# Kernel tuning notes

Hardware: AMD Instinct MI355X
Metric: run time of the kernel (lower is better)

The kernel has to match this reference:

```python
import jax, jax.numpy as jnp
import numpy as np

B, T, C, H = 2, 2048, 1024, 16
HD = C // H  # head dim = 64


def setup_inputs() -> dict:
    key = jax.random.key(0)
    ks = jax.random.split(key, 5)
    s = 1.0 / np.sqrt(C)
    return {
        "x": jax.random.normal(ks[0], (B, T, C), dtype=jnp.float32),
        "W_attn": jax.random.normal(ks[1], (3 * C, C), dtype=jnp.float32) * s,
        "b_attn": jax.random.normal(ks[2], (3 * C,), dtype=jnp.float32) * 0.02,
        "W_proj": jax.random.normal(ks[3], (C, C), dtype=jnp.float32) * s,
        "b_proj": jax.random.normal(ks[4], (C,), dtype=jnp.float32) * 0.02,
    }


def reference(x, W_attn, b_attn, W_proj, b_proj):
    Bx, Tx, Cx = x.shape
    # fused QKV projection (torch Linear: x @ W.T + b)
    qkv = x @ W_attn.T + b_attn                      # [B,T,3C]
    q, k, v = jnp.split(qkv, 3, axis=-1)
    # [B,T,C] -> [B,H,T,hd]
    q = q.reshape(Bx, Tx, H, HD).transpose(0, 2, 1, 3)
    k = k.reshape(Bx, Tx, H, HD).transpose(0, 2, 1, 3)
    v = v.reshape(Bx, Tx, H, HD).transpose(0, 2, 1, 3)
    scale = 1.0 / np.sqrt(HD)
    att = jnp.einsum('bhqd,bhkd->bhqk', q, k) * scale  # [B,H,T,T]
    causal = jnp.tril(jnp.ones((Tx, Tx), dtype=bool))
    att = jnp.where(causal[None, None], att, -jnp.inf)
    att = jax.nn.softmax(att, axis=-1)
    y = jnp.einsum('bhqk,bhkd->bhqd', att, v)          # [B,H,T,hd]
    y = y.transpose(0, 2, 1, 3).reshape(Bx, Tx, Cx)
    return y @ W_proj.T + b_proj
```

## Files before the change

kernel.cpp:

```cpp
#include <hip/hip_runtime.h>

typedef unsigned short ushort_t;
typedef __bf16 bf16x8 __attribute__((ext_vector_type(8)));
typedef float f32x4 __attribute__((ext_vector_type(4)));
typedef unsigned u32x4 __attribute__((ext_vector_type(4)));

__device__ inline ushort_t f2bf(float f) {
  unsigned int u = __builtin_bit_cast(unsigned int, f);
  u += 0x7fff + ((u >> 16) & 1);
  return (ushort_t)(u >> 16);
}

__device__ inline unsigned pk_bf(float a, float b) {
  unsigned r;
  asm("v_cvt_pk_bf16_f32 %0, %1, %2" : "=v"(r) : "v"(a), "v"(b));
  return r;
}

__device__ inline void async_ld16(const ushort_t* g, const ushort_t* l) {
  __builtin_amdgcn_global_load_lds(
      (const __attribute__((address_space(1))) void*)g,
      (__attribute__((address_space(3))) void*)l, 16, 0, 0);
}

template <int IMM>
__device__ inline void waitcnt_barrier() {
  asm volatile("" ::: "memory");
  __builtin_amdgcn_s_waitcnt(IMM);
  __builtin_amdgcn_s_barrier();
  asm volatile("" ::: "memory");
}

__global__ void cvt_all(const float* __restrict__ x, const float* __restrict__ wa,
                        const float* __restrict__ wp, ushort_t* __restrict__ xb,
                        ushort_t* __restrict__ wab, ushort_t* __restrict__ wpb) {
  int i = blockIdx.x * 256 + threadIdx.x;
  const float* src;
  ushort_t* dst;
  int off;
  if (i < 1048576) { src = x; dst = xb; off = i; }
  else if (i < 1835008) { src = wa; dst = wab; off = i - 1048576; }
  else { src = wp; dst = wpb; off = i - 1835008; }
  float4 f = ((const float4*)src)[off];
  unsigned long long p = (unsigned long long)f2bf(f.x)
      | ((unsigned long long)f2bf(f.y) << 16)
      | ((unsigned long long)f2bf(f.z) << 32)
      | ((unsigned long long)f2bf(f.w) << 48);
  ((unsigned long long*)dst)[off] = p;
}

template <int BM, int BN, int IM, int JN, int MODE, int TPB>
__global__ __launch_bounds__(TPB) void gemm_bt(
    const ushort_t* __restrict__ A, const ushort_t* __restrict__ B,
    const float* __restrict__ bias, float* __restrict__ Cf,
    ushort_t* __restrict__ Cb, ushort_t* __restrict__ vtb,
    int M, int N, int K, int ldc, float qscale) {
  constexpr int NWN = BN / (JN * 16);
  constexpr int NL = (BM + BN) * 32 / (TPB * 8);
  constexpr int WIMM = 0x0F70 | NL;
  __shared__ __align__(16) ushort_t As[3][BM * 32];
  __shared__ __align__(16) ushort_t Bs[3][BN * 32];
  const int tid = threadIdx.x;
  const int wave = tid >> 6, lane = tid & 63;
  const int quad = lane >> 4, l16 = lane & 15;
  const int wr = wave / NWN, wc = wave % NWN;
  const int wm = wr * IM * 16, wn = wc * JN * 16;
  const int m0 = blockIdx.y * BM, n0 = blockIdx.x * BN;
  const ushort_t* Ag = A + (size_t)m0 * K;
  const ushort_t* Bg = B + (size_t)n0 * K;
  const int slot = (quad ^ ((l16 >> 1) & 3)) * 8;
  f32x4 acc[IM][JN] = {};

  auto stage = [&](int kt, int bsel) {
    int k0 = kt * 32;
#pragma unroll
    for (int p = 0; p < BM * 4 / TPB; ++p) {
      int ci = p * TPB + tid;
      int row = ci >> 2, ch = (ci & 3) ^ ((ci >> 3) & 3);
      async_ld16(Ag + (size_t)row * K + k0 + ch * 8, As[bsel] + (p * TPB + wave * 64) * 8);
    }
#pragma unroll
    for (int p = 0; p < BN * 4 / TPB; ++p) {
      int ci = p * TPB + tid;
      int row = ci >> 2, ch = (ci & 3) ^ ((ci >> 3) & 3);
      async_ld16(Bg + (size_t)row * K + k0 + ch * 8, Bs[bsel] + (p * TPB + wave * 64) * 8);
    }
  };

  const int KT = K / 32;
  stage(0, 0);
  stage(1, 1);
  for (int kt = 0; kt < KT; ++kt) {
    waitcnt_barrier<WIMM>();
    if (kt + 2 < KT) stage(kt + 2, (kt + 2) % 3);
    const ushort_t* Ac = As[kt % 3];
    const ushort_t* Bc = Bs[kt % 3];
    bf16x8 af[IM], bfr[JN];
#pragma unroll
    for (int i = 0; i < IM; ++i)
      af[i] = *(const bf16x8*)(Ac + (wm + i * 16 + l16) * 32 + slot);
#pragma unroll
    for (int j = 0; j < JN; ++j)
      bfr[j] = *(const bf16x8*)(Bc + (wn + j * 16 + l16) * 32 + slot);
#pragma unroll
    for (int i = 0; i < IM; ++i)
#pragma unroll
      for (int j = 0; j < JN; ++j)
        acc[i][j] = __builtin_amdgcn_mfma_f32_16x16x32_bf16(af[i], bfr[j], acc[i][j], 0, 0, 0);
  }

  if (MODE == 1 && n0 >= 2048) {
#pragma unroll
    for (int j = 0; j < JN; ++j) {
      int col = n0 + wn + j * 16 + l16;
      int cv = col - 2048;
      float bv = bias[col];
      size_t rowbase = ((size_t)(cv >> 6)) * 64 + (cv & 63);
#pragma unroll
      for (int i = 0; i < IM; ++i) {
        int rowb = m0 + wm + i * 16 + quad * 4;
        int bb = rowb >> 11, t = rowb & 2047;
        uint2 pp;
        pp.x = pk_bf(acc[i][j][0] + bv, acc[i][j][1] + bv);
        pp.y = pk_bf(acc[i][j][2] + bv, acc[i][j][3] + bv);
        *(uint2*)(vtb + (((size_t)bb * 1024 + rowbase) * 2048 + t)) = pp;
      }
    }
    return;
  }
#pragma unroll
  for (int j = 0; j < JN; ++j) {
    int col = n0 + wn + j * 16 + l16;
    float bv = bias[col];
    float sc = (MODE == 1 && col < 1024) ? qscale : 1.0f;
#pragma unroll
    for (int i = 0; i < IM; ++i)
#pragma unroll
      for (int r = 0; r < 4; ++r) {
        int row = m0 + wm + i * 16 + quad * 4 + r;
        float v = (acc[i][j][r] + bv) * sc;
        if (MODE == 1)
          Cb[(size_t)row * ldc + col] = f2bf(v);
        else
          Cf[(size_t)row * ldc + col] = v;
      }
  }
}

__global__ __launch_bounds__(512, 4) void flash8(
    const ushort_t* __restrict__ qk, const ushort_t* __restrict__ vt,
    ushort_t* __restrict__ y) {
  __shared__ __align__(16) ushort_t Kb[4][4096];
  __shared__ __align__(16) ushort_t Vb[4][4096];
  const int tid = threadIdx.x, wave = tid >> 6, lane = tid & 63;
  const int quad = lane >> 4, l16 = lane & 15;
  const int r7 = l16 & 7;
  const int fK = (l16 & 3) | (((l16 >> 2) & 1) << 2);
  const int kbase = (16 * (l16 >> 2) + (l16 & 3)) * 64;
  const int xx = blockIdx.x, bh = blockIdx.y;
  const int Q = (bh < 16) ? (15 - xx) : xx;
  const int b = bh >> 4, h = bh & 15;
  const int bT = b * 2048;
  const int qw = Q * 128 + wave * 16;

  bf16x8 qf[2];
  {
    const ushort_t* qrow = qk + (size_t)(bT + qw + l16) * 2048 + h * 64 + quad * 8;
    qf[0] = *(const bf16x8*)(qrow);
    qf[1] = *(const bf16x8*)(qrow + 32);
  }

  auto stage = [&](int kt, int bsel) {
    int k0 = kt * 64;
    int row = tid >> 3;
    int chk = (tid & 7) ^ ((row & 3) | (((row >> 4) & 1) << 2));
    int chv = (tid & 7) ^ (row & 7);
    async_ld16(qk + (size_t)(bT + k0 + row) * 2048 + 1024 + h * 64 + chk * 8,
               Kb[bsel] + wave * 512);
    async_ld16(vt + (size_t)(bh * 64 + row) * 2048 + k0 + chv * 8,
               Vb[bsel] + wave * 512);
  };

  f32x4 o[4] = {};
  float lac0 = 0.f, lac1 = 0.f;
  const int KT = 2 * Q + 2;

  stage(0, 0);
  stage(1, 1);
  if (KT > 2) stage(2, 2);
  for (int kt = 0; kt < KT; ++kt) {
    const int cur = kt & 3;
    int ahead = KT - 1 - kt;
    if (ahead >= 2)      waitcnt_barrier<0x0F74>();
    else if (ahead == 1) waitcnt_barrier<0x0F72>();
    else                 waitcnt_barrier<0x0F70>();
    if (kt + 3 < KT) stage(kt + 3, (kt + 3) & 3);
    const ushort_t* Kc = Kb[cur];
    const ushort_t* Vc = Vb[cur];
    bf16x8 kf[4][2];
#pragma unroll
    for (int j = 0; j < 4; ++j)
#pragma unroll
      for (int ks = 0; ks < 2; ++ks)
        kf[j][ks] = *(const bf16x8*)(Kc + kbase + j * 256 + (((ks * 4 + quad) ^ fK) * 8));
    f32x4 s[4] = {};
#pragma unroll
    for (int ks = 0; ks < 2; ++ks)
#pragma unroll
      for (int j = 0; j < 4; ++j)
        s[j] = __builtin_amdgcn_mfma_f32_16x16x32_bf16(kf[j][ks], qf[ks], s[j], 0, 0, 0);
    if (kt >= KT - 2) {
      int qloc = qw + l16;
#pragma unroll
      for (int j = 0; j < 4; ++j)
#pragma unroll
        for (int r = 0; r < 4; ++r)
          if (kt * 64 + quad * 16 + j * 4 + r > qloc) s[j][r] = -1e30f;
    }
#pragma unroll
    for (int j = 0; j < 4; ++j)
#pragma unroll
      for (int r = 0; r < 4; ++r) {
        float pv = exp2f(s[j][r]);
        s[j][r] = pv;
        if (j & 1) lac1 += pv; else lac0 += pv;
      }
    bf16x8 pf[2];
#pragma unroll
    for (int ks = 0; ks < 2; ++ks) {
      u32x4 w;
      w[0] = pk_bf(s[2 * ks][0], s[2 * ks][1]);
      w[1] = pk_bf(s[2 * ks][2], s[2 * ks][3]);
      w[2] = pk_bf(s[2 * ks + 1][0], s[2 * ks + 1][1]);
      w[3] = pk_bf(s[2 * ks + 1][2], s[2 * ks + 1][3]);
      pf[ks] = __builtin_bit_cast(bf16x8, w);
    }
#pragma unroll
    for (int ks = 0; ks < 2; ++ks)
#pragma unroll
      for (int j = 0; j < 4; ++j) {
        bf16x8 vf = *(const bf16x8*)(Vc + (j * 16 + l16) * 64 + (((ks + 2 * quad) ^ r7) * 8));
        o[j] = __builtin_amdgcn_mfma_f32_16x16x32_bf16(vf, pf[ks], o[j], 0, 0, 0);
      }
  }

  {
    float l = lac0 + lac1;
    l += __shfl_xor(l, 16, 64);
    l += __shfl_xor(l, 32, 64);
    float inv = 1.f / l;
    size_t row = (size_t)(bT + qw + l16);
#pragma unroll
    for (int j = 0; j < 4; ++j) {
      uint2 pp;
      pp.x = pk_bf(o[j][0] * inv, o[j][1] * inv);
      pp.y = pk_bf(o[j][2] * inv, o[j][3] * inv);
      *(uint2*)(y + row * 1024 + h * 64 + j * 16 + quad * 4) = pp;
    }
  }
}

extern "C" void kernel_launch(void* const* d_in, const int* in_sizes, int n_in,
                              void* d_out, int out_size, void* d_ws, size_t ws_size,
                              hipStream_t stream) {
  const float* x  = (const float*)d_in[0];
  const float* Wa = (const float*)d_in[1];
  const float* ba = (const float*)d_in[2];
  const float* Wp = (const float*)d_in[3];
  const float* bp = (const float*)d_in[4];
  float* out = (float*)d_out;
  char* ws = (char*)d_ws;
  ushort_t* xb  = (ushort_t*)(ws);
  ushort_t* Wab = (ushort_t*)(ws + 8388608);
  ushort_t* Wpb = (ushort_t*)(ws + 14680064);
  ushort_t* qkb = (ushort_t*)(ws + 16777216);
  ushort_t* yb  = (ushort_t*)(ws + 33554432);
  ushort_t* vtb = (ushort_t*)(ws + 41943040);

  cvt_all<<<8192, 256, 0, stream>>>(x, Wa, Wp, xb, Wab, Wpb);
  gemm_bt<128, 128, 4, 2, 1, 512><<<dim3(24, 32), 512, 0, stream>>>(
      xb, Wab, ba, nullptr, qkb, vtb, 4096, 3072, 1024, 2048, 0.18033688011112042f);
  flash8<<<dim3(16, 32), 512, 0, stream>>>(qkb, vtb, yb);
  gemm_bt<64, 64, 2, 2, 0, 256><<<dim3(16, 64), 256, 0, stream>>>(
      yb, Wpb, bp, out, nullptr, nullptr, 4096, 1024, 1024, 1024, 1.0f);
}
```

Before: 181.2 us.

## Process two key tiles per barrier with double-buffered superstages in flash kernel

The flash attention loop now groups two 64-key tiles into one superstage. It double-buffers superstages instead of keeping a 4-deep single-tile ring, so there is one barrier and full wait per two tiles instead of one per tile. It also raises wave priority around the compute section with s_setprio. The trade-off is shallower prefetch: the next superstage loads while the current one computes, but a full vmcnt(0) wait can expose latency. LDS use is unchanged.

```diff
diff --git a/kernel.cpp b/kernel.cpp
--- a/kernel.cpp
+++ b/kernel.cpp
@@ -147,11 +147,11 @@
   }
 }
 
-__global__ __launch_bounds__(512, 4) void flash8(
+__global__ __launch_bounds__(512, 4) void flash9(
     const ushort_t* __restrict__ qk, const ushort_t* __restrict__ vt,
     ushort_t* __restrict__ y) {
-  __shared__ __align__(16) ushort_t Kb[4][4096];
-  __shared__ __align__(16) ushort_t Vb[4][4096];
+  __shared__ __align__(16) ushort_t Kb[2][2][4096];
+  __shared__ __align__(16) ushort_t Vb[2][2][4096];
   const int tid = threadIdx.x, wave = tid >> 6, lane = tid & 63;
   const int quad = lane >> 4, l16 = lane & 15;
   const int r7 = l16 & 7;
@@ -170,78 +170,83 @@
     qf[1] = *(const bf16x8*)(qrow + 32);
   }
 
-  auto stage = [&](int kt, int bsel) {
+  auto stage1 = [&](int kt, int bsel, int u) {
     int k0 = kt * 64;
     int row = tid >> 3;
     int chk = (tid & 7) ^ ((row & 3) | (((row >> 4) & 1) << 2));
     int chv = (tid & 7) ^ (row & 7);
     async_ld16(qk + (size_t)(bT + k0 + row) * 2048 + 1024 + h * 64 + chk * 8,
-               Kb[bsel] + wave * 512);
+               Kb[bsel][u] + wave * 512);
     async_ld16(vt + (size_t)(bh * 64 + row) * 2048 + k0 + chv * 8,
-               Vb[bsel] + wave * 512);
+               Vb[bsel][u] + wave * 512);
   };
+  auto stageS = [&](int s, int bsel) { stage1(2 * s, bsel, 0); stage1(2 * s + 1, bsel, 1); };
 
   f32x4 o[4] = {};
   float lac0 = 0.f, lac1 = 0.f;
-  const int KT = 2 * Q + 2;
-
-  stage(0, 0);
-  stage(1, 1);
-  if (KT > 2) stage(2, 2);
-  for (int kt = 0; kt < KT; ++kt) {
-    const int cur = kt & 3;
-    int ahead = KT - 1 - kt;
-    if (ahead >= 2)      waitcnt_barrier<0x0F74>();
-    else if (ahead == 1) waitcnt_barrier<0x0F72>();
-    else                 waitcnt_barrier<0x0F70>();
-    if (kt + 3 < KT) stage(kt + 3, (kt + 3) & 3);
-    const ushort_t* Kc = Kb[cur];
-    const ushort_t* Vc = Vb[cur];
-    bf16x8 kf[4][2];
-#pragma unroll
-    for (int j = 0; j < 4; ++j)
+  const int NS = Q + 1;
+
+  stageS(0, 0);
+  for (int s = 0; s < NS; ++s) {
+    const int cur = s & 1;
+    waitcnt_barrier<0x0F70>();
+    if (s + 1 < NS) stageS(s + 1, cur ^ 1);
+    __builtin_amdgcn_s_setprio(1);
+    bf16x8 pf[2][2];
+#pragma unroll
+    for (int u = 0; u < 2; ++u) {
+      const ushort_t* Kc = Kb[cur][u];
+      const ushort_t* Vc = Vb[cur][u];
+      bf16x8 kf[4][2];
+#pragma unroll
+      for (int j = 0; j < 4; ++j)
+#pragma unroll
+        for (int ks = 0; ks < 2; ++ks)
+          kf[j][ks] = *(const bf16x8*)(Kc + kbase + j * 256 + (((ks * 4 + quad) ^ fK) * 8));
+      f32x4 sr[4] = {};
 #pragma unroll
       for (int ks = 0; ks < 2; ++ks)
-        kf[j][ks] = *(const bf16x8*)(Kc + kbase + j * 256 + (((ks * 4 + quad) ^ fK) * 8));
-    f32x4 s[4] = {};
-#pragma unroll
-    for (int ks = 0; ks < 2; ++ks)
+#pragma unroll
+        for (int j = 0; j < 4; ++j)
+          sr[j] = __builtin_amdgcn_mfma_f32_16x16x32_bf16(kf[j][ks], qf[ks], sr[j], 0, 0, 0);
+      if (s == NS - 1) {
+        int qloc = qw + l16;
+        int kt0 = (2 * s + u) * 64;
+#pragma unroll
+        for (int j = 0; j < 4; ++j)
+#pragma unroll
+          for (int r = 0; r < 4; ++r)
+            if (kt0 + quad * 16 + j * 4 + r > qloc) sr[j][r] = -1e30f;
+      }
 #pragma unroll
       for (int j = 0; j < 4; ++j)
-        s[j] = __builtin_amdgcn_mfma_f32_16x16x32_bf16(kf[j][ks], qf[ks], s[j], 0, 0, 0);
-    if (kt >= KT - 2) {
-      int qloc = qw + l16;
+#pragma unroll
+        for (int r = 0; r < 4; ++r)
+          sr[j][r] = exp2f(sr[j][r]);
+#pragma unroll
+      for (int ks = 0; ks < 2; ++ks) {
+        u32x4 w;
+        w[0] = pk_bf(sr[2 * ks][0], sr[2 * ks][1]);
+        w[1] = pk_bf(sr[2 * ks][2], sr[2 * ks][3]);
+        w[2] = pk_bf(sr[2 * ks + 1][0], sr[2 * ks + 1][1]);
+        w[3] = pk_bf(sr[2 * ks + 1][2], sr[2 * ks + 1][3]);
+        pf[u][ks] = __builtin_bit_cast(bf16x8, w);
+      }
 #pragma unroll
       for (int j = 0; j < 4; ++j)
 #pragma unroll
-        for (int r = 0; r < 4; ++r)
-          if (kt * 64 + quad * 16 + j * 4 + r > qloc) s[j][r] = -1e30f;
-    }
-#pragma unroll
-    for (int j = 0; j < 4; ++j)
-#pragma unroll
-      for (int r = 0; r < 4; ++r) {
-        float pv = exp2f(s[j][r]);
-        s[j][r] = pv;
-        if (j & 1) lac1 += pv; else lac0 += pv;
-      }
-    bf16x8 pf[2];
-#pragma unroll
-    for (int ks = 0; ks < 2; ++ks) {
-      u32x4 w;
-      w[0] = pk_bf(s[2 * ks][0], s[2 * ks][1]);
-      w[1] = pk_bf(s[2 * ks][2], s[2 * ks][3]);
-      w[2] = pk_bf(s[2 * ks + 1][0], s[2 * ks + 1][1]);
-      w[3] = pk_bf(s[2 * ks + 1][2], s[2 * ks + 1][3]);
-      pf[ks] = __builtin_bit_cast(bf16x8, w);
-    }
-#pragma unroll
-    for (int ks = 0; ks < 2; ++ks)
-#pragma unroll
-      for (int j = 0; j < 4; ++j) {
-        bf16x8 vf = *(const bf16x8*)(Vc + (j * 16 + l16) * 64 + (((ks + 2 * quad) ^ r7) * 8));
-        o[j] = __builtin_amdgcn_mfma_f32_16x16x32_bf16(vf, pf[ks], o[j], 0, 0, 0);
-      }
+        for (int r = 0; r < 4; ++r) {
+          if (j & 1) lac1 += sr[j][r]; else lac0 += sr[j][r];
+        }
+#pragma unroll
+      for (int ks = 0; ks < 2; ++ks)
+#pragma unroll
+        for (int j = 0; j < 4; ++j) {
+          bf16x8 vf = *(const bf16x8*)(Vc + (j * 16 + l16) * 64 + (((ks + 2 * quad) ^ r7) * 8));
+          o[j] = __builtin_amdgcn_mfma_f32_16x16x32_bf16(vf, pf[u][ks], o[j], 0, 0, 0);
+        }
+    }
+    __builtin_amdgcn_s_setprio(0);
   }
 
   {
@@ -280,7 +285,7 @@
   cvt_all<<<8192, 256, 0, stream>>>(x, Wa, Wp, xb, Wab, Wpb);
   gemm_bt<128, 128, 4, 2, 1, 512><<<dim3(24, 32), 512, 0, stream>>>(
       xb, Wab, ba, nullptr, qkb, vtb, 4096, 3072, 1024, 2048, 0.18033688011112042f);
-  flash8<<<dim3(16, 32), 512, 0, stream>>>(qkb, vtb, yb);
+  flash9<<<dim3(16, 32), 512, 0, stream>>>(qkb, vtb, yb);
   gemm_bt<64, 64, 2, 2, 0, 256><<<dim3(16, 64), 256, 0, stream>>>(
       yb, Wpb, bp, out, nullptr, nullptr, 4096, 1024, 1024, 1024, 1.0f);
 }
```

New measurement: 178.4 us. Within noise of the previous version (-1.5%).
